# Optimization experiments

Hardware: AMD Instinct MI355X
Metric: run time of the kernel (lower is better)

## Reference

```python
import jax, jax.numpy as jnp
import numpy as np
from jax.ops import segment_sum, segment_max

H = 64          # hidden_dim
HEADS = 4       # GAT heads (concat=False -> mean over heads)
N_VAR = 500_000
N_EMP = 3_000
N_SHIFT = 30_000
N_CON = 50_000
E_SD = 960_000
E_VE = 500_000
E_VS = 500_000
F_EMP, F_SHIFT, F_VAR, F_CON = 32, 24, 19, 5


def setup_inputs() -> dict:
    key = jax.random.key(0)
    ks = jax.random.split(key, 32)
    def g(i, shape):
        return jax.random.normal(ks[i], shape, jnp.float32) * 0.05
    return dict(
        x_emp=jax.random.normal(ks[0], (N_EMP, F_EMP), jnp.float32),
        x_shift=jax.random.normal(ks[1], (N_SHIFT, F_SHIFT), jnp.float32),
        x_var=jax.random.normal(ks[2], (N_VAR, F_VAR), jnp.float32),
        x_con=jax.random.normal(ks[3], (N_CON, F_CON), jnp.float32),
        W_emp=g(4, (F_EMP, H)), b_emp=jnp.zeros((H,), jnp.float32),
        W_shift=g(5, (F_SHIFT, H)), b_shift=jnp.zeros((H,), jnp.float32),
        W_var=g(6, (F_VAR, H)), b_var=jnp.zeros((H,), jnp.float32),
        W_con=g(7, (F_CON, H)), b_con=jnp.zeros((H,), jnp.float32),
        gat_W=g(8, (H, HEADS * H)), gat_att_src=g(9, (HEADS, H)),
        gat_att_dst=g(10, (HEADS, H)), gat_b=jnp.zeros((H,), jnp.float32),
        injW_emp=g(11, (H, H)), injb_emp=jnp.zeros((H,), jnp.float32),
        injW_shift=g(12, (H, H)), injb_shift=jnp.zeros((H,), jnp.float32),
        qW_emp=g(13, (H, H)), kW_emp=g(14, (H, H)),
        qW_shift=g(15, (H, H)), kW_shift=g(16, (H, H)),
        fuseW=g(17, (3 * H, H)), fuseb=jnp.zeros((H,), jnp.float32),
        sd_src=jax.random.randint(ks[18], (E_SD,), 0, N_SHIFT),
        sd_dst=jax.random.randint(ks[19], (E_SD,), 0, N_SHIFT),
        ve_var=jax.random.randint(ks[20], (E_VE,), 0, N_VAR),
        ve_emp=jax.random.randint(ks[21], (E_VE,), 0, N_EMP),
        vs_var=jax.random.randint(ks[22], (E_VS,), 0, N_VAR),
        vs_shift=jax.random.randint(ks[23], (E_VS,), 0, N_SHIFT),
    )


def _gat(h, W, att_src, att_dst, bias, src, dst):
    # PyG GATConv, heads=HEADS, concat=False, no self-loops, eval mode (no dropout)
    n = h.shape[0]
    x = (h @ W).reshape(n, HEADS, H)                    # [S, heads, H]
    a_s = jnp.einsum('nhd,hd->nh', x, att_src)          # [S, heads]
    a_d = jnp.einsum('nhd,hd->nh', x, att_dst)
    e = jax.nn.leaky_relu(a_s[src] + a_d[dst], 0.2)     # [E, heads]
    m = segment_max(e, dst, num_segments=n)
    ex = jnp.exp(e - m[dst])
    z = segment_sum(ex, dst, num_segments=n)
    alpha = ex / jnp.maximum(z[dst], 1e-16)             # scatter-softmax per dst node
    out = segment_sum(x[src] * alpha[:, :, None], dst, num_segments=n)
    return out.mean(axis=1) + bias                      # concat=False -> head mean


def _inject(h_var, h_ent, injW, injb, qW, kW, dst, src):
    # gather Q/K/V per edge -> dot score -> segment softmax over variables -> scatter-sum
    scale = jnp.sqrt(jnp.float32(H))
    vals = (h_ent @ injW + injb)[src]                   # [E, H]
    q = (h_var @ qW)[dst]                               # [E, H]
    k = (h_ent @ kW)[src]                               # [E, H]
    s = jnp.sum(q * k, axis=-1) / scale                 # [E]
    m = segment_max(s, dst, num_segments=N_VAR)
    e = jnp.exp(s - m[dst])
    z = jnp.maximum(segment_sum(e, dst, num_segments=N_VAR), 1e-9)
    alpha = e / z[dst]
    return segment_sum(vals * alpha[:, None], dst, num_segments=N_VAR)


def reference(x_emp, x_shift, x_var, x_con,
              W_emp, b_emp, W_shift, b_shift, W_var, b_var, W_con, b_con,
              gat_W, gat_att_src, gat_att_dst, gat_b,
              injW_emp, injb_emp, injW_shift, injb_shift,
              qW_emp, kW_emp, qW_shift, kW_shift, fuseW, fuseb,
              sd_src, sd_dst, ve_var, ve_emp, vs_var, vs_shift):
    # Stage 0: project all node types to hidden_dim
    h_emp = jax.nn.relu(x_emp @ W_emp + b_emp)
    h_shift = jax.nn.relu(x_shift @ W_shift + b_shift)
    h_var = jax.nn.relu(x_var @ W_var + b_var)
    h_con = jax.nn.relu(x_con @ W_con + b_con)  # projected but unused downstream
    # Stage 1: one HeteroConv layer = GAT on Shift same_day edges, relu + residual
    gat_out = _gat(h_shift, gat_W, gat_att_src, gat_att_dst, gat_b, sd_src, sd_dst)
    h_shift = jax.nn.relu(gat_out) + h_shift
    # Stage 2: semantic injection into variable nodes
    msg_e = _inject(h_var, h_emp, injW_emp, injb_emp, qW_emp, kW_emp, ve_var, ve_emp)
    msg_s = _inject(h_var, h_shift, injW_shift, injb_shift, qW_shift, kW_shift, vs_var, vs_shift)
    fused = jnp.concatenate([h_var, msg_e, msg_s], axis=-1)  # [N_var, 3H]
    h_var_new = jax.nn.relu(fused @ fuseW + fuseb)
    return jnp.sqrt(jnp.sum(h_var_new * h_var_new, axis=-1))  # L2 norm pseudo-scores
```

## Files before the change

### kernel.cpp

```cpp
#include <hip/hip_runtime.h>
#include <math.h>

#define NEMP   3000
#define NSHIFT 30000
#define NVAR   500000
#define ESD    960000
#define EVE    500000
#define EVS    500000
#define NT_CNT (NSHIFT + NVAR + NVAR)
#define ET_ALL (ESD + EVE + EVS)

#define NBUCK  959
#define NBLK0  256
#define CHUNK  7657
#define SSTRIDE 7664

#define S2CAP  384
#define GCAP   1536

typedef __attribute__((ext_vector_type(8))) short short8;
typedef __attribute__((ext_vector_type(4))) float f32x4;

__device__ __forceinline__ unsigned short f2bf(float x) {
  unsigned u = __float_as_uint(x);
  unsigned r = (u + 0x7FFFu + ((u >> 16) & 1u)) >> 16;
  return (unsigned short)r;
}
__device__ __forceinline__ float bf2f(unsigned short u) {
  return __uint_as_float((unsigned)u << 16);
}
__device__ __forceinline__ int swz(int r, int f) {
  return (((f >> 3) ^ (r & 7)) << 3) | (f & 7);
}
__device__ __forceinline__ int kvoff(int j, int isV) {
  return ((j >> 2) << 3) | (isV << 2) | (j & 3);
}

__device__ __forceinline__ void edge_decode(int i,
    const int* __restrict__ sd_dst, const int* __restrict__ sd_src,
    const int* __restrict__ ve_var, const int* __restrict__ ve_emp,
    const int* __restrict__ vs_var, const int* __restrict__ vs_shift,
    int& b, unsigned& packed) {
  if (i < ESD)            { int d = sd_dst[i]; b = d >> 6; packed = (unsigned)(d & 63) | ((unsigned)sd_src[i] << 11); }
  else if (i < ESD + EVE) { int j = i - ESD; int d = ve_var[j]; b = 469 + (d >> 11); packed = (unsigned)(d & 2047) | ((unsigned)ve_emp[j] << 11); }
  else                    { int j = i - ESD - EVE; int d = vs_var[j]; b = 714 + (d >> 11); packed = (unsigned)(d & 2047) | ((unsigned)vs_shift[j] << 11); }
}

__device__ __forceinline__ void qkfold_body(const float* __restrict__ qW,
    const float* __restrict__ kW, float* __restrict__ W2,
    unsigned short* __restrict__ W2frag) {
  int j = threadIdx.x & 63;
  int fq = threadIdx.x >> 6;
  for (int ff = 0; ff < 16; ++ff) {
    int f = fq * 16 + ff;
    float acc = 0.0f;
    #pragma unroll
    for (int d = 0; d < 64; ++d) acc = fmaf(qW[j * 64 + d], kW[f * 64 + d], acc);
    float val = 0.125f * acc;
    if (W2) W2[f * 64 + j] = val;
    if (W2frag) {
      int kb = f >> 5;
      int lane = (((f & 31) >> 3) << 4) | (j & 15);
      int ntile = j >> 4;
      W2frag[((((ntile << 1) + kb) * 64 + lane) << 3) | (f & 7)] = f2bf(val);
    }
  }
}

__global__ __launch_bounds__(256) void prep_bin_kernel(
    const float* __restrict__ qWe, const float* __restrict__ kWe,
    const float* __restrict__ qWs, const float* __restrict__ kWs,
    const float* __restrict__ fuseW, const float* __restrict__ gat_W,
    const float* __restrict__ att_src, const float* __restrict__ att_dst,
    const float* __restrict__ W_var, const float* __restrict__ injW_s,
    float* __restrict__ W2e, unsigned short* __restrict__ W2sb,
    unsigned short* __restrict__ injWsb,
    unsigned short* __restrict__ fuseWb,
    float* __restrict__ w_as, float* __restrict__ w_ad,
    unsigned short* __restrict__ Wrb, unsigned short* __restrict__ Wvb,
    const int* __restrict__ sd_dst, const int* __restrict__ sd_src,
    const int* __restrict__ ve_var, const int* __restrict__ ve_emp,
    const int* __restrict__ vs_var, const int* __restrict__ vs_shift,
    unsigned* __restrict__ staging, int* __restrict__ table, int* __restrict__ btot) {
  __shared__ int hist[NBUCK];
  __shared__ int sums[256];
  int t = threadIdx.x;
  int bx = blockIdx.x;
  if (bx < 7) {
    if (bx == 0) { qkfold_body(qWe, kWe, W2e, nullptr); return; }
    if (bx == 1) { qkfold_body(qWs, kWs, nullptr, W2sb); return; }
    if (bx == 2) {
      for (int linear = t; linear < 192 * 64; linear += 256) {
        int i    = linear & 7;
        int lane = (linear >> 3) & 63;
        int g    = linear >> 9;
        int kb   = g % 6, nt = g / 6;
        int k = kb * 32 + (lane >> 4) * 8 + i;
        int n = nt * 16 + (lane & 15);
        fuseWb[linear] = f2bf(fuseW[k * 64 + n]);
      }
      return;
    }
    if (bx == 3) {
      int h = t >> 6, f = t & 63;
      float as = 0.0f, ad = 0.0f;
      #pragma unroll
      for (int d = 0; d < 64; ++d) {
        float wv = gat_W[f * 256 + h * 64 + d];
        as = fmaf(wv, att_src[h * 64 + d], as);
        ad = fmaf(wv, att_dst[h * 64 + d], ad);
      }
      w_as[f * 4 + h] = as;
      w_ad[f * 4 + h] = ad;
      return;
    }
    if (bx == 4) {
      for (int linear = t; linear < 4 * 8 * 64 * 8; linear += 256) {
        int i    = linear & 7;
        int lane = (linear >> 3) & 63;
        int g    = linear >> 9;
        int kb   = g & 7, nt = g >> 3;
        int k = kb * 32 + ((lane >> 4) << 3) + i;
        int j = nt * 16 + (lane & 15);
        Wrb[linear] = f2bf(0.25f * gat_W[(k & 63) * 256 + (k >> 6) * 64 + j]);
      }
      return;
    }
    if (bx == 5) {
      for (int linear = t; linear < 4 * 64 * 8; linear += 256) {
        int i    = linear & 7;
        int lane = (linear >> 3) & 63;
        int nt   = linear >> 9;
        int k = ((lane >> 4) << 3) + i;
        int j = nt * 16 + (lane & 15);
        Wvb[linear] = (k < 19) ? f2bf(W_var[k * 64 + j]) : (unsigned short)0;
      }
      return;
    }
    for (int linear = t; linear < 4 * 2 * 64 * 8; linear += 256) {
      int i    = linear & 7;
      int lane = (linear >> 3) & 63;
      int g    = linear >> 9;
      int kb   = g & 1, nt = g >> 1;
      int k = kb * 32 + ((lane >> 4) << 3) + i;
      int j = nt * 16 + (lane & 15);
      injWsb[linear] = f2bf(injW_s[k * 64 + j]);
    }
    return;
  }
  int blk = bx - 7;
  int e0 = blk * CHUNK;
  int e1 = min(e0 + CHUNK, ET_ALL);
  int sbase = blk * SSTRIDE;
  for (int i = t; i < NBUCK; i += 256) hist[i] = 0;
  __syncthreads();
  for (int i = e0 + t; i < e1; i += 256) {
    int b; unsigned pk;
    edge_decode(i, sd_dst, sd_src, ve_var, ve_emp, vs_var, vs_shift, b, pk);
    atomicAdd(&hist[b], 1);
  }
  __syncthreads();
  for (int i = t; i < NBUCK; i += 256) { int h = hist[i]; if (h) atomicAdd(&btot[i], h); }
  int base = t * 4, v[4], s = 0;
  #pragma unroll
  for (int k = 0; k < 4; ++k) { int i = base + k; v[k] = (i < NBUCK) ? hist[i] : 0; s += v[k]; }
  sums[t] = s; __syncthreads();
  for (int o = 1; o < 256; o <<= 1) {
    int add = (t >= o) ? sums[t - o] : 0;
    __syncthreads(); sums[t] += add; __syncthreads();
  }
  int run = sums[t] - s;
  #pragma unroll
  for (int k = 0; k < 4; ++k) {
    int i = base + k;
    if (i < NBUCK) { hist[i] = run; table[i * NBLK0 + blk] = sbase + run; run += v[k]; }
  }
  if (t == 0) table[NBUCK * NBLK0 + blk] = sbase + (e1 - e0);
  __syncthreads();
  for (int i = e0 + t; i < e1; i += 256) {
    int b; unsigned pk;
    edge_decode(i, sd_dst, sd_src, ve_var, ve_emp, vs_var, vs_shift, b, pk);
    int pos = sbase + atomicAdd(&hist[b], 1);
    staging[pos] = pk;
  }
}

__global__ __launch_bounds__(1024) void bstart_kernel(const int* __restrict__ btot,
                                                      int* __restrict__ bstart) {
  __shared__ int sd[1024];
  int t = threadIdx.x;
  int v = (t < NBUCK) ? btot[t] : 0;
  sd[t] = v; __syncthreads();
  for (int o = 1; o < 1024; o <<= 1) {
    int add = (t >= o) ? sd[t - o] : 0;
    __syncthreads(); sd[t] += add; __syncthreads();
  }
  if (t < NBUCK) bstart[t] = sd[t] - v;
  if (t == NBUCK - 1) bstart[NBUCK] = sd[t];
}

template<int F>
__device__ __forceinline__ void proj_body(const float* __restrict__ x,
    const float* __restrict__ W, const float* __restrict__ b,
    float* __restrict__ out, int blk, int N) {
  int n = __builtin_amdgcn_readfirstlane((int)(blk * 4 + (threadIdx.x >> 6)));
  int j = threadIdx.x & 63;
  if (n >= N) return;
  const float* xr = x + (size_t)n * F;
  float acc = b[j];
  #pragma unroll
  for (int f = 0; f < F; ++f) acc = fmaf(xr[f], W[f * 64 + j], acc);
  out[(size_t)n * 64 + j] = fmaxf(acc, 0.0f);
}

__global__ __launch_bounds__(256) void csr_proj_kernel(
    const unsigned* __restrict__ staging, const int* __restrict__ table,
    const int* __restrict__ bstart, int* __restrict__ row, int* __restrict__ elist,
    const float* __restrict__ x_emp, const float* __restrict__ W_emp,
    const float* __restrict__ b_emp, float* __restrict__ h_emp,
    const float* __restrict__ x_shift, const float* __restrict__ W_shift,
    const float* __restrict__ b_shift, float* __restrict__ h_sh0,
    unsigned short* __restrict__ h_sh0b,
    const float* __restrict__ w_as, const float* __restrict__ w_ad,
    float* __restrict__ a_s, float* __restrict__ a_d) {
  __shared__ int hist[2048];
  __shared__ int sums[256];
  int bx = blockIdx.x, t = threadIdx.x;
  if (bx >= NBUCK) {
    int blk = bx - NBUCK;
    if (blk < 750) { proj_body<32>(x_emp, W_emp, b_emp, h_emp, blk, NEMP); return; }
    int nb = blk - 750;
    int n = __builtin_amdgcn_readfirstlane((int)(nb * 4 + (t >> 6)));
    int j = t & 63;
    if (n >= NSHIFT) return;
    const float* xr = x_shift + (size_t)n * 24;
    float acc = b_shift[j];
    #pragma unroll
    for (int f = 0; f < 24; ++f) acc = fmaf(xr[f], W_shift[f * 64 + j], acc);
    float h = fmaxf(acc, 0.0f);
    h_sh0[(size_t)n * 64 + j] = h;
    h_sh0b[(size_t)n * 64 + j] = f2bf(h);
    const float4 was4 = *(const float4*)(w_as + j * 4);
    const float4 wad4 = *(const float4*)(w_ad + j * 4);
    float s0 = h * was4.x, s1 = h * was4.y, s2 = h * was4.z, s3 = h * was4.w;
    float d0 = h * wad4.x, d1 = h * wad4.y, d2 = h * wad4.z, d3 = h * wad4.w;
    #pragma unroll
    for (int o = 32; o > 0; o >>= 1) {
      s0 += __shfl_xor(s0, o); s1 += __shfl_xor(s1, o);
      s2 += __shfl_xor(s2, o); s3 += __shfl_xor(s3, o);
      d0 += __shfl_xor(d0, o); d1 += __shfl_xor(d1, o);
      d2 += __shfl_xor(d2, o); d3 += __shfl_xor(d3, o);
    }
    if (j == 0) {
      *(float4*)(a_s + n * 4) = make_float4(s0, s1, s2, s3);
      *(float4*)(a_d + n * 4) = make_float4(d0, d1, d2, d3);
    }
    return;
  }
  int b = bx;
  int s0 = table[b * NBLK0 + t];
  int s1 = table[(b + 1) * NBLK0 + t];
  for (int i = t; i < 2048; i += 256) hist[i] = 0;
  __syncthreads();
  for (int p = s0; p < s1; ++p) atomicAdd(&hist[staging[p] & 2047u], 1);
  __syncthreads();
  int keyBase, kcount;
  if (b < 469)      { keyBase = b * 64;                     kcount = min(64,   30000  - b * 64); }
  else if (b < 714) { int lb = b - 469; keyBase = 30000  + lb * 2048; kcount = min(2048, 500000 - lb * 2048); }
  else              { int lb = b - 714; keyBase = 530000 + lb * 2048; kcount = min(2048, 500000 - lb * 2048); }
  int bs = bstart[b];
  int base = t * 8, v[8], s = 0;
  #pragma unroll
  for (int k = 0; k < 8; ++k) { int i = base + k; v[k] = (i < kcount) ? hist[i] : 0; s += v[k]; }
  sums[t] = s; __syncthreads();
  for (int o = 1; o < 256; o <<= 1) {
    int add = (t >= o) ? sums[t - o] : 0;
    __syncthreads(); sums[t] += add; __syncthreads();
  }
  int run = sums[t] - s;
  #pragma unroll
  for (int k = 0; k < 8; ++k) {
    int i = base + k;
    if (i < kcount) { hist[i] = run; row[keyBase + i] = bs + run; run += v[k]; }
  }
  if (b == NBUCK - 1 && t == 0) row[NT_CNT] = bstart[NBUCK];
  __syncthreads();
  for (int p = s0; p < s1; ++p) {
    unsigned pr = staging[p];
    int pos = bs + atomicAdd(&hist[pr & 2047u], 1);
    elist[pos] = (int)(pr >> 11);
  }
}

__global__ __launch_bounds__(512) void gat_linemp_kernel(
    const float* __restrict__ h_sh0, const unsigned short* __restrict__ h_sh0b,
    const float* __restrict__ a_s, const float* __restrict__ a_d,
    const int* __restrict__ row, const int* __restrict__ elist,
    const unsigned short* __restrict__ Wrb, const float* __restrict__ gat_b,
    const unsigned short* __restrict__ W2sb, const unsigned short* __restrict__ injWsb,
    const float* __restrict__ injb_s,
    unsigned short* __restrict__ KVs,
    const float* __restrict__ h_emp, const float* __restrict__ injW_e,
    const float* __restrict__ injb_e, const float* __restrict__ W2e,
    unsigned short* __restrict__ KVe) {
  __shared__ unsigned short aggTn[32][256];
  __shared__ __attribute__((aligned(16))) unsigned short hb[32][64];
  __shared__ int elG[GCAP];
  __shared__ int rowLocG[33];
  int tid = threadIdx.x;
  int bx = blockIdx.x;
  if (bx >= 938) {
    int b = bx - 938;
    const float *W, *bias; int isV, nb;
    if (b < 375) { W = injW_e; bias = injb_e;  isV = 1; nb = b; }
    else         { W = W2e;    bias = nullptr; isV = 0; nb = b - 375; }
    int n = __builtin_amdgcn_readfirstlane((int)(nb * 8 + (tid >> 6)));
    int j = tid & 63;
    if (n >= NEMP) return;
    const float* hr = h_emp + (size_t)n * 64;
    float acc = bias ? bias[j] : 0.0f;
    #pragma unroll
    for (int f = 0; f < 64; ++f) acc = fmaf(hr[f], W[f * 64 + j], acc);
    KVe[(n << 7) | kvoff(j, isV)] = f2bf(acc);
    return;
  }
  int lane = tid & 63;
  int w = __builtin_amdgcn_readfirstlane((int)(tid >> 6));
  int blockStart = bx * 32;
  if (tid < 33) rowLocG[tid] = row[min(blockStart + tid, NSHIFT)];
  __syncthreads();
  int baseG = rowLocG[0];
  int lenG = min(rowLocG[32] - baseG, GCAP);
  for (int i = tid; i < lenG; i += 512) elG[i] = elist[baseG + i];
  __syncthreads();

  for (int k = 0; k < 4; ++k) {
    int c = w * 4 + k;
    int n = blockStart + c;
    float4 ad4 = make_float4(0.f, 0.f, 0.f, 0.f);
    if (n < NSHIFT) ad4 = *(const float4*)(a_d + (n << 2));
    int lb = rowLocG[c] - baseG, le = rowLocG[c + 1] - baseG;
    float g0 = 0, g1 = 0, g2 = 0, g3 = 0, z0 = 0, z1 = 0, z2 = 0, z3 = 0;
    int p = lb;
    for (; p + 2 <= le; p += 2) {
      int s0 = elG[p], s1 = elG[p + 1];
      const float4 asA = *(const float4*)(a_s + (s0 << 2));
      const float4 asB = *(const float4*)(a_s + (s1 << 2));
      float hvA = bf2f(h_sh0b[(s0 << 6) | lane]);
      float hvB = bf2f(h_sh0b[(s1 << 6) | lane]);
      float a0 = asA.x + ad4.x, a1 = asA.y + ad4.y, a2 = asA.z + ad4.z, a3 = asA.w + ad4.w;
      float b0 = asB.x + ad4.x, b1 = asB.y + ad4.y, b2 = asB.z + ad4.z, b3 = asB.w + ad4.w;
      a0 = a0 > 0.f ? a0 : 0.2f * a0;  a1 = a1 > 0.f ? a1 : 0.2f * a1;
      a2 = a2 > 0.f ? a2 : 0.2f * a2;  a3 = a3 > 0.f ? a3 : 0.2f * a3;
      b0 = b0 > 0.f ? b0 : 0.2f * b0;  b1 = b1 > 0.f ? b1 : 0.2f * b1;
      b2 = b2 > 0.f ? b2 : 0.2f * b2;  b3 = b3 > 0.f ? b3 : 0.2f * b3;
      float xA0 = __expf(a0), xA1 = __expf(a1), xA2 = __expf(a2), xA3 = __expf(a3);
      float xB0 = __expf(b0), xB1 = __expf(b1), xB2 = __expf(b2), xB3 = __expf(b3);
      z0 += xA0 + xB0; z1 += xA1 + xB1; z2 += xA2 + xB2; z3 += xA3 + xB3;
      g0 = fmaf(xA0, hvA, fmaf(xB0, hvB, g0));
      g1 = fmaf(xA1, hvA, fmaf(xB1, hvB, g1));
      g2 = fmaf(xA2, hvA, fmaf(xB2, hvB, g2));
      g3 = fmaf(xA3, hvA, fmaf(xB3, hvB, g3));
    }
    if (p < le) {
      int s0 = elG[p];
      const float4 asA = *(const float4*)(a_s + (s0 << 2));
      float hvA = bf2f(h_sh0b[(s0 << 6) | lane]);
      float a0 = asA.x + ad4.x, a1 = asA.y + ad4.y, a2 = asA.z + ad4.z, a3 = asA.w + ad4.w;
      a0 = a0 > 0.f ? a0 : 0.2f * a0;  a1 = a1 > 0.f ? a1 : 0.2f * a1;
      a2 = a2 > 0.f ? a2 : 0.2f * a2;  a3 = a3 > 0.f ? a3 : 0.2f * a3;
      float xA0 = __expf(a0), xA1 = __expf(a1), xA2 = __expf(a2), xA3 = __expf(a3);
      z0 += xA0; z1 += xA1; z2 += xA2; z3 += xA3;
      g0 = fmaf(xA0, hvA, g0); g1 = fmaf(xA1, hvA, g1);
      g2 = fmaf(xA2, hvA, g2); g3 = fmaf(xA3, hvA, g3);
    }
    aggTn[c][swz(c, lane)]       = f2bf(g0 / fmaxf(z0, 1e-16f));
    aggTn[c][swz(c, 64 + lane)]  = f2bf(g1 / fmaxf(z1, 1e-16f));
    aggTn[c][swz(c, 128 + lane)] = f2bf(g2 / fmaxf(z2, 1e-16f));
    aggTn[c][swz(c, 192 + lane)] = f2bf(g3 / fmaxf(z3, 1e-16f));
  }
  __syncthreads();

  {
    int mtile = w >> 2, ntile = w & 3;
    int row16 = lane & 15, blk4 = lane >> 4;
    int mrow = mtile * 16 + row16;
    f32x4 acc = {0.f, 0.f, 0.f, 0.f};
    #pragma unroll
    for (int kb = 0; kb < 8; ++kb) {
      short8 a = *(const short8*)&aggTn[mrow][swz(mrow, kb * 32 + blk4 * 8)];
      short8 bfr = *(const short8*)(Wrb + (((ntile * 8 + kb) * 64 + lane) << 3));
      acc = __builtin_amdgcn_mfma_f32_16x16x32_bf16(a, bfr, acc, 0, 0, 0);
    }
    int j = ntile * 16 + row16;
    float gb = gat_b[j];
    #pragma unroll
    for (int r = 0; r < 4; ++r) {
      int nl = mtile * 16 + blk4 * 4 + r;
      int node = blockStart + nl;
      float o = 0.0f;
      if (node < NSHIFT)
        o = fmaxf(acc[r] + gb, 0.0f) + h_sh0[(size_t)node * 64 + j];
      hb[nl][swz(nl, j)] = f2bf(o);
    }
  }
  __syncthreads();

  {
    int mat = w & 1;
    int mtile = (w >> 1) & 1;
    int npair = w >> 2;
    const unsigned short* Wfrag = mat ? injWsb : W2sb;
    int row16 = lane & 15, blk4 = lane >> 4;
    int mrow = mtile * 16 + row16;
    #pragma unroll
    for (int tt = 0; tt < 2; ++tt) {
      int ntile = npair * 2 + tt;
      f32x4 acc = {0.f, 0.f, 0.f, 0.f};
      #pragma unroll
      for (int kb = 0; kb < 2; ++kb) {
        short8 a = *(const short8*)&hb[mrow][swz(mrow, kb * 32 + blk4 * 8)];
        short8 bfr = *(const short8*)(Wfrag + (((ntile * 2 + kb) * 64 + lane) << 3));
        acc = __builtin_amdgcn_mfma_f32_16x16x32_bf16(a, bfr, acc, 0, 0, 0);
      }
      int j = ntile * 16 + row16;
      float bias = mat ? injb_s[j] : 0.0f;
      #pragma unroll
      for (int r = 0; r < 4; ++r) {
        int node = blockStart + mtile * 16 + blk4 * 4 + r;
        if (node < NSHIFT)
          KVs[(node << 7) | kvoff(j, mat)] = f2bf(acc[r] + bias);
      }
    }
  }
}

__global__ __launch_bounds__(512) void stage2_kernel(
    const float* __restrict__ x_var, const unsigned short* __restrict__ Wvb,
    const float* __restrict__ b_var,
    const unsigned short* __restrict__ KVe, const int* __restrict__ ve_row,
    const unsigned short* __restrict__ KVs, const int* __restrict__ vs_row,
    const int* __restrict__ elist,
    const unsigned short* __restrict__ fuseWb, const float* __restrict__ fuseb,
    float* __restrict__ out, int N) {
  __shared__ __attribute__((aligned(16))) unsigned short fTn[64][192];
  __shared__ __attribute__((aligned(16))) unsigned short xb[64][40];
  __shared__ int elE[S2CAP], elS[S2CAP];
  __shared__ int rowLocE[65], rowLocS[65];
  __shared__ float ssq2[64][2];
  int tid = threadIdx.x;
  int lane = tid & 63;
  int w = __builtin_amdgcn_readfirstlane((int)(tid >> 6));
  int sl = lane & 15;
  int blockStart = blockIdx.x * 64;

  if (tid < 65) {
    int nn = min(blockStart + tid, N);
    rowLocE[tid] = ve_row[nn];
    rowLocS[tid] = vs_row[nn];
  }
  {
    int r = tid >> 3, k = tid & 7;
    int n = blockStart + r;
    bool act = (n < N);
    const float* xr = x_var + (size_t)n * 19;
    float v0 = act ? xr[k] : 0.0f;
    float v1 = act ? xr[8 + k] : 0.0f;
    float v2 = (act && k < 3) ? xr[16 + k] : 0.0f;
    xb[r][k] = f2bf(v0);
    xb[r][8 + k] = f2bf(v1);
    xb[r][16 + k] = (k < 3) ? f2bf(v2) : (unsigned short)0;
    xb[r][24 + k] = 0;
  }
  __syncthreads();

  int baseE = rowLocE[0], baseS = rowLocS[0];
  int lenE = min(rowLocE[64] - baseE, S2CAP);
  int lenS = min(rowLocS[64] - baseS, S2CAP);
  for (int i = tid; i < lenE; i += 512) elE[i] = elist[baseE + i];
  for (int i = tid; i < lenS; i += 512) elS[i] = elist[baseS + i];

  {
    int mtile = w >> 1;
    int mrow = mtile * 16 + sl;
    short8 a = *(const short8*)&xb[mrow][(lane >> 4) * 8];
    #pragma unroll
    for (int t = 0; t < 2; ++t) {
      int ntile = (w & 1) * 2 + t;
      short8 bfr = *(const short8*)(Wvb + ((ntile * 64 + lane) << 3));
      f32x4 acc = {0.f, 0.f, 0.f, 0.f};
      acc = __builtin_amdgcn_mfma_f32_16x16x32_bf16(a, bfr, acc, 0, 0, 0);
      int dim = ntile * 16 + sl;
      float bv = b_var[dim];
      #pragma unroll
      for (int r = 0; r < 4; ++r) {
        int node = mtile * 16 + (lane >> 4) * 4 + r;
        fTn[node][swz(node, dim)] = f2bf(fmaxf(acc[r] + bv, 0.0f));
      }
    }
  }
  __syncthreads();

  {
    int g = lane >> 4;
    int sl4 = sl << 2;
    int sl8 = sl << 3;
    #pragma unroll
    for (int k = 0; k < 4; ++k) {
      int task = k * 4 + g;
      bool typS = task >= 8;
      int c = w * 8 + (task & 7);
      const unsigned short* KV = typS ? KVs : KVe;
      const int* rowLoc = typS ? rowLocS : rowLocE;
      const int* elL = typS ? elS : elE;
      int bb = typS ? baseS : baseE;
      int outBase = typS ? 128 : 64;
      int lb = rowLoc[c] - bb, le = rowLoc[c + 1] - bb;
      int deg = le - lb;
      ushort4 msgb = make_ushort4(0, 0, 0, 0);
      if (deg == 1) {
        msgb = *(const ushort4*)(KV + ((elL[lb] << 7) | sl8 | 4));
      } else if (deg > 1) {
        const ushort4 hu = *(const ushort4*)&fTn[c][swz(c, sl4)];
        float4 hv = make_float4(bf2f(hu.x), bf2f(hu.y), bf2f(hu.z), bf2f(hu.w));
        float z = 0.0f;
        float4 acc = make_float4(0.f, 0.f, 0.f, 0.f);
        int p = lb;
        for (; p + 2 <= le; p += 2) {
          short8 kv0 = *(const short8*)(KV + ((elL[p] << 7) | sl8));
          short8 kv1 = *(const short8*)(KV + ((elL[p + 1] << 7) | sl8));
          float p0 = hv.x * bf2f((unsigned short)kv0[0]) + hv.y * bf2f((unsigned short)kv0[1])
                   + hv.z * bf2f((unsigned short)kv0[2]) + hv.w * bf2f((unsigned short)kv0[3]);
          float p1 = hv.x * bf2f((unsigned short)kv1[0]) + hv.y * bf2f((unsigned short)kv1[1])
                   + hv.z * bf2f((unsigned short)kv1[2]) + hv.w * bf2f((unsigned short)kv1[3]);
          p0 += __shfl_xor(p0, 1); p1 += __shfl_xor(p1, 1);
          p0 += __shfl_xor(p0, 2); p1 += __shfl_xor(p1, 2);
          p0 += __shfl_xor(p0, 4); p1 += __shfl_xor(p1, 4);
          p0 += __shfl_xor(p0, 8); p1 += __shfl_xor(p1, 8);
          float e0 = __expf(p0), e1 = __expf(p1);
          z += e0 + e1;
          acc.x = fmaf(e0, bf2f((unsigned short)kv0[4]), fmaf(e1, bf2f((unsigned short)kv1[4]), acc.x));
          acc.y = fmaf(e0, bf2f((unsigned short)kv0[5]), fmaf(e1, bf2f((unsigned short)kv1[5]), acc.y));
          acc.z = fmaf(e0, bf2f((unsigned short)kv0[6]), fmaf(e1, bf2f((unsigned short)kv1[6]), acc.z));
          acc.w = fmaf(e0, bf2f((unsigned short)kv0[7]), fmaf(e1, bf2f((unsigned short)kv1[7]), acc.w));
        }
        if (p < le) {
          short8 kv0 = *(const short8*)(KV + ((elL[p] << 7) | sl8));
          float p0 = hv.x * bf2f((unsigned short)kv0[0]) + hv.y * bf2f((unsigned short)kv0[1])
                   + hv.z * bf2f((unsigned short)kv0[2]) + hv.w * bf2f((unsigned short)kv0[3]);
          p0 += __shfl_xor(p0, 1); p0 += __shfl_xor(p0, 2);
          p0 += __shfl_xor(p0, 4); p0 += __shfl_xor(p0, 8);
          float e0 = __expf(p0);
          z += e0;
          acc.x = fmaf(e0, bf2f((unsigned short)kv0[4]), acc.x);
          acc.y = fmaf(e0, bf2f((unsigned short)kv0[5]), acc.y);
          acc.z = fmaf(e0, bf2f((unsigned short)kv0[6]), acc.z);
          acc.w = fmaf(e0, bf2f((unsigned short)kv0[7]), acc.w);
        }
        float inv = 1.0f / fmaxf(z, 1e-9f);
        msgb = make_ushort4(f2bf(acc.x * inv), f2bf(acc.y * inv),
                            f2bf(acc.z * inv), f2bf(acc.w * inv));
      }
      *(ushort4*)&fTn[c][swz(c, outBase + sl4)] = msgb;
    }
  }
  __syncthreads();

  {
    int mtile = w >> 1;
    int row16 = lane & 15, blk = lane >> 4;
    int mrow = mtile * 16 + row16;
    float nodeSS[4] = {0.f, 0.f, 0.f, 0.f};
    #pragma unroll
    for (int t = 0; t < 2; ++t) {
      int ntile = (w & 1) * 2 + t;
      f32x4 acc = {0.f, 0.f, 0.f, 0.f};
      #pragma unroll
      for (int kb = 0; kb < 6; ++kb) {
        short8 a = *(const short8*)&fTn[mrow][swz(mrow, kb * 32 + blk * 8)];
        short8 bfr = *(const short8*)(fuseWb + (((ntile * 6 + kb) * 64 + lane) << 3));
        acc = __builtin_amdgcn_mfma_f32_16x16x32_bf16(a, bfr, acc, 0, 0, 0);
      }
      float fb = fuseb[ntile * 16 + row16];
      #pragma unroll
      for (int r = 0; r < 4; ++r) {
        float v = fmaxf(acc[r] + fb, 0.0f);
        float vv = v * v;
        vv += __shfl_xor(vv, 1); vv += __shfl_xor(vv, 2);
        vv += __shfl_xor(vv, 4); vv += __shfl_xor(vv, 8);
        nodeSS[r] += vv;
      }
    }
    if (row16 == 0) {
      #pragma unroll
      for (int r = 0; r < 4; ++r)
        ssq2[mtile * 16 + blk * 4 + r][w & 1] = nodeSS[r];
    }
  }
  __syncthreads();
  if (tid < 64) {
    int n = blockStart + tid;
    if (n < N) out[n] = sqrtf(ssq2[tid][0] + ssq2[tid][1]);
  }
}

extern "C" void kernel_launch(void* const* d_in, const int* in_sizes, int n_in,
                              void* d_out, int out_size, void* d_ws, size_t ws_size,
                              hipStream_t stream) {
  const float* x_emp   = (const float*)d_in[0];
  const float* x_shift = (const float*)d_in[1];
  const float* x_var   = (const float*)d_in[2];
  const float* W_emp   = (const float*)d_in[4];
  const float* b_emp   = (const float*)d_in[5];
  const float* W_shift = (const float*)d_in[6];
  const float* b_shift = (const float*)d_in[7];
  const float* W_var   = (const float*)d_in[8];
  const float* b_var   = (const float*)d_in[9];
  const float* gat_W   = (const float*)d_in[12];
  const float* att_s   = (const float*)d_in[13];
  const float* att_d   = (const float*)d_in[14];
  const float* gat_b   = (const float*)d_in[15];
  const float* injW_e  = (const float*)d_in[16];
  const float* injb_e  = (const float*)d_in[17];
  const float* injW_s  = (const float*)d_in[18];
  const float* injb_s  = (const float*)d_in[19];
  const float* qW_e    = (const float*)d_in[20];
  const float* kW_e    = (const float*)d_in[21];
  const float* qW_s    = (const float*)d_in[22];
  const float* kW_s    = (const float*)d_in[23];
  const float* fuseW   = (const float*)d_in[24];
  const float* fuseb   = (const float*)d_in[25];
  const int* sd_src  = (const int*)d_in[26];
  const int* sd_dst  = (const int*)d_in[27];
  const int* ve_var  = (const int*)d_in[28];
  const int* ve_emp  = (const int*)d_in[29];
  const int* vs_var  = (const int*)d_in[30];
  const int* vs_shift= (const int*)d_in[31];
  float* out = (float*)d_out;

  char* base = (char*)d_ws;
  size_t off = 0;
  auto A = [&](size_t nbytes) -> void* {
    void* r = base + off;
    off = (off + nbytes + 255) & ~(size_t)255;
    return r;
  };
  float* h_emp = (float*)A((size_t)NEMP * 64 * 4);
  float* h_sh0 = (float*)A((size_t)NSHIFT * 64 * 4);
  unsigned short* h_sh0b = (unsigned short*)A((size_t)NSHIFT * 64 * 2);
  float* a_s   = (float*)A((size_t)NSHIFT * 4 * 4);
  float* a_d   = (float*)A((size_t)NSHIFT * 4 * 4);
  unsigned short* KVe = (unsigned short*)A((size_t)NEMP * 128 * 2);
  unsigned short* KVs = (unsigned short*)A((size_t)NSHIFT * 128 * 2);
  float* W2e   = (float*)A((size_t)64 * 64 * 4);
  unsigned short* W2sb   = (unsigned short*)A((size_t)4 * 2 * 64 * 8 * 2);
  unsigned short* injWsb = (unsigned short*)A((size_t)4 * 2 * 64 * 8 * 2);
  float* w_as  = (float*)A((size_t)64 * 4 * 4);
  float* w_ad  = (float*)A((size_t)64 * 4 * 4);
  unsigned short* fuseWb = (unsigned short*)A((size_t)192 * 64 * 2);
  unsigned short* Wrb    = (unsigned short*)A((size_t)256 * 64 * 2);
  unsigned short* Wvb    = (unsigned short*)A((size_t)4 * 64 * 8 * 2);
  int* row_all = (int*)A((size_t)(NT_CNT + 1) * 4);
  int* el_all  = (int*)A((size_t)ET_ALL * 4);
  unsigned* staging = (unsigned*)A((size_t)NBLK0 * SSTRIDE * 4);
  int* table   = (int*)A((size_t)(NBUCK + 1) * NBLK0 * 4);
  int* bstart  = (int*)A((size_t)(NBUCK + 1) * 4);
  int* btot    = (int*)A((size_t)NBUCK * 4);

  hipMemsetAsync(btot, 0, (size_t)NBUCK * 4, stream);

  prep_bin_kernel<<<7 + NBLK0, 256, 0, stream>>>(
      qW_e, kW_e, qW_s, kW_s, fuseW, gat_W, att_s, att_d, W_var, injW_s,
      W2e, W2sb, injWsb, fuseWb, w_as, w_ad, Wrb, Wvb,
      sd_dst, sd_src, ve_var, ve_emp, vs_var, vs_shift,
      staging, table, btot);

  bstart_kernel<<<1, 1024, 0, stream>>>(btot, bstart);

  csr_proj_kernel<<<NBUCK + 750 + 7500, 256, 0, stream>>>(
      staging, table, bstart, row_all, el_all,
      x_emp, W_emp, b_emp, h_emp,
      x_shift, W_shift, b_shift, h_sh0, h_sh0b,
      w_as, w_ad, a_s, a_d);

  gat_linemp_kernel<<<938 + 750, 512, 0, stream>>>(
      h_sh0, h_sh0b, a_s, a_d, row_all, el_all, Wrb, gat_b,
      W2sb, injWsb, injb_s, KVs,
      h_emp, injW_e, injb_e, W2e, KVe);

  stage2_kernel<<<(NVAR + 63) / 64, 512, 0, stream>>>(x_var, Wvb, b_var,
      KVe, row_all + NSHIFT,
      KVs, row_all + NSHIFT + NVAR,
      el_all, fuseWb, fuseb, out, NVAR);
}
```

Measured before the change: 282.9 us.

## Drop bucket-total pass by deriving bucket starts from staging offsets

Result: faster. 271.4 us (-4.1%).

```diff
diff --git a/kernel.cpp b/kernel.cpp
--- a/kernel.cpp
+++ b/kernel.cpp
@@ -14,6 +14,7 @@
 #define NBLK0  256
 #define CHUNK  7657
 #define SSTRIDE 7664
+#define SBIAS  250152960
 
 #define S2CAP  384
 #define GCAP   1536
@@ -81,9 +82,11 @@
     const int* __restrict__ sd_dst, const int* __restrict__ sd_src,
     const int* __restrict__ ve_var, const int* __restrict__ ve_emp,
     const int* __restrict__ vs_var, const int* __restrict__ vs_shift,
-    unsigned* __restrict__ staging, int* __restrict__ table, int* __restrict__ btot) {
+    unsigned* __restrict__ staging, int* __restrict__ table) {
   __shared__ int hist[NBUCK];
   __shared__ int sums[256];
+  __shared__ unsigned pkc[CHUNK];
+  __shared__ unsigned short bkc[CHUNK];
   int t = threadIdx.x;
   int bx = blockIdx.x;
   if (bx < 7) {
@@ -157,10 +160,11 @@
   for (int i = e0 + t; i < e1; i += 256) {
     int b; unsigned pk;
     edge_decode(i, sd_dst, sd_src, ve_var, ve_emp, vs_var, vs_shift, b, pk);
+    pkc[i - e0] = pk;
+    bkc[i - e0] = (unsigned short)b;
     atomicAdd(&hist[b], 1);
   }
   __syncthreads();
-  for (int i = t; i < NBUCK; i += 256) { int h = hist[i]; if (h) atomicAdd(&btot[i], h); }
   int base = t * 4, v[4], s = 0;
   #pragma unroll
   for (int k = 0; k < 4; ++k) { int i = base + k; v[k] = (i < NBUCK) ? hist[i] : 0; s += v[k]; }
@@ -178,25 +182,10 @@
   if (t == 0) table[NBUCK * NBLK0 + blk] = sbase + (e1 - e0);
   __syncthreads();
   for (int i = e0 + t; i < e1; i += 256) {
-    int b; unsigned pk;
-    edge_decode(i, sd_dst, sd_src, ve_var, ve_emp, vs_var, vs_shift, b, pk);
+    int b = bkc[i - e0];
     int pos = sbase + atomicAdd(&hist[b], 1);
-    staging[pos] = pk;
-  }
-}
-
-__global__ __launch_bounds__(1024) void bstart_kernel(const int* __restrict__ btot,
-                                                      int* __restrict__ bstart) {
-  __shared__ int sd[1024];
-  int t = threadIdx.x;
-  int v = (t < NBUCK) ? btot[t] : 0;
-  sd[t] = v; __syncthreads();
-  for (int o = 1; o < 1024; o <<= 1) {
-    int add = (t >= o) ? sd[t - o] : 0;
-    __syncthreads(); sd[t] += add; __syncthreads();
-  }
-  if (t < NBUCK) bstart[t] = sd[t] - v;
-  if (t == NBUCK - 1) bstart[NBUCK] = sd[t];
+    staging[pos] = pkc[i - e0];
+  }
 }
 
 template<int F>
@@ -215,11 +204,11 @@
 
 __global__ __launch_bounds__(256) void csr_proj_kernel(
     const unsigned* __restrict__ staging, const int* __restrict__ table,
-    const int* __restrict__ bstart, int* __restrict__ row, int* __restrict__ elist,
+    int* __restrict__ row, int* __restrict__ elist,
     const float* __restrict__ x_emp, const float* __restrict__ W_emp,
     const float* __restrict__ b_emp, float* __restrict__ h_emp,
     const float* __restrict__ x_shift, const float* __restrict__ W_shift,
-    const float* __restrict__ b_shift, float* __restrict__ h_sh0,
+    const float* __restrict__ b_shift,
     unsigned short* __restrict__ h_sh0b,
     const float* __restrict__ w_as, const float* __restrict__ w_ad,
     float* __restrict__ a_s, float* __restrict__ a_d) {
@@ -238,7 +227,6 @@
     #pragma unroll
     for (int f = 0; f < 24; ++f) acc = fmaf(xr[f], W_shift[f * 64 + j], acc);
     float h = fmaxf(acc, 0.0f);
-    h_sh0[(size_t)n * 64 + j] = h;
     h_sh0b[(size_t)n * 64 + j] = f2bf(h);
     const float4 was4 = *(const float4*)(w_as + j * 4);
     const float4 wad4 = *(const float4*)(w_ad + j * 4);
@@ -260,6 +248,17 @@
   int b = bx;
   int s0 = table[b * NBLK0 + t];
   int s1 = table[(b + 1) * NBLK0 + t];
+  sums[t] = s0; __syncthreads();
+  for (int o = 128; o > 0; o >>= 1) { if (t < o) sums[t] += sums[t + o]; __syncthreads(); }
+  int bs = sums[0] - SBIAS;
+  int totAll = 0;
+  if (b == NBUCK - 1) {
+    __syncthreads();
+    sums[t] = s1; __syncthreads();
+    for (int o = 128; o > 0; o >>= 1) { if (t < o) sums[t] += sums[t + o]; __syncthreads(); }
+    totAll = sums[0] - SBIAS;
+  }
+  __syncthreads();
   for (int i = t; i < 2048; i += 256) hist[i] = 0;
   __syncthreads();
   for (int p = s0; p < s1; ++p) atomicAdd(&hist[staging[p] & 2047u], 1);
@@ -268,7 +267,6 @@
   if (b < 469)      { keyBase = b * 64;                     kcount = min(64,   30000  - b * 64); }
   else if (b < 714) { int lb = b - 469; keyBase = 30000  + lb * 2048; kcount = min(2048, 500000 - lb * 2048); }
   else              { int lb = b - 714; keyBase = 530000 + lb * 2048; kcount = min(2048, 500000 - lb * 2048); }
-  int bs = bstart[b];
   int base = t * 8, v[8], s = 0;
   #pragma unroll
   for (int k = 0; k < 8; ++k) { int i = base + k; v[k] = (i < kcount) ? hist[i] : 0; s += v[k]; }
@@ -283,7 +281,7 @@
     int i = base + k;
     if (i < kcount) { hist[i] = run; row[keyBase + i] = bs + run; run += v[k]; }
   }
-  if (b == NBUCK - 1 && t == 0) row[NT_CNT] = bstart[NBUCK];
+  if (b == NBUCK - 1 && t == 0) row[NT_CNT] = totAll;
   __syncthreads();
   for (int p = s0; p < s1; ++p) {
     unsigned pr = staging[p];
@@ -293,7 +291,7 @@
 }
 
 __global__ __launch_bounds__(512) void gat_linemp_kernel(
-    const float* __restrict__ h_sh0, const unsigned short* __restrict__ h_sh0b,
+    const unsigned short* __restrict__ h_sh0b,
     const float* __restrict__ a_s, const float* __restrict__ a_d,
     const int* __restrict__ row, const int* __restrict__ elist,
     const unsigned short* __restrict__ Wrb, const float* __restrict__ gat_b,
@@ -400,7 +398,7 @@
       int node = blockStart + nl;
       float o = 0.0f;
       if (node < NSHIFT)
-        o = fmaxf(acc[r] + gb, 0.0f) + h_sh0[(size_t)node * 64 + j];
+        o = fmaxf(acc[r] + gb, 0.0f) + bf2f(h_sh0b[((size_t)node << 6) | j]);
       hb[nl][swz(nl, j)] = f2bf(o);
     }
   }
@@ -646,7 +644,6 @@
     return r;
   };
   float* h_emp = (float*)A((size_t)NEMP * 64 * 4);
-  float* h_sh0 = (float*)A((size_t)NSHIFT * 64 * 4);
   unsigned short* h_sh0b = (unsigned short*)A((size_t)NSHIFT * 64 * 2);
   float* a_s   = (float*)A((size_t)NSHIFT * 4 * 4);
   float* a_d   = (float*)A((size_t)NSHIFT * 4 * 4);
@@ -664,27 +661,21 @@
   int* el_all  = (int*)A((size_t)ET_ALL * 4);
   unsigned* staging = (unsigned*)A((size_t)NBLK0 * SSTRIDE * 4);
   int* table   = (int*)A((size_t)(NBUCK + 1) * NBLK0 * 4);
-  int* bstart  = (int*)A((size_t)(NBUCK + 1) * 4);
-  int* btot    = (int*)A((size_t)NBUCK * 4);
-
-  hipMemsetAsync(btot, 0, (size_t)NBUCK * 4, stream);
 
   prep_bin_kernel<<<7 + NBLK0, 256, 0, stream>>>(
       qW_e, kW_e, qW_s, kW_s, fuseW, gat_W, att_s, att_d, W_var, injW_s,
       W2e, W2sb, injWsb, fuseWb, w_as, w_ad, Wrb, Wvb,
       sd_dst, sd_src, ve_var, ve_emp, vs_var, vs_shift,
-      staging, table, btot);
-
-  bstart_kernel<<<1, 1024, 0, stream>>>(btot, bstart);
+      staging, table);
 
   csr_proj_kernel<<<NBUCK + 750 + 7500, 256, 0, stream>>>(
-      staging, table, bstart, row_all, el_all,
+      staging, table, row_all, el_all,
       x_emp, W_emp, b_emp, h_emp,
-      x_shift, W_shift, b_shift, h_sh0, h_sh0b,
+      x_shift, W_shift, b_shift, h_sh0b,
       w_as, w_ad, a_s, a_d);
 
   gat_linemp_kernel<<<938 + 750, 512, 0, stream>>>(
-      h_sh0, h_sh0b, a_s, a_d, row_all, el_all, Wrb, gat_b,
+      h_sh0b, a_s, a_d, row_all, el_all, Wrb, gat_b,
       W2sb, injWsb, injb_s, KVs,
       h_emp, injW_e, injb_e, W2e, KVe);
 
```
